# Optimization experiments

Hardware: AMD Instinct MI355X
Metric: run time of the kernel (lower is better)

Reference implementation:

```python
import jax, jax.numpy as jnp
import numpy as np

N_NODES = 50000
N_EDGES = 800000
IN_CH = 128
HIDDEN = 32
HEADS = 4
NEG_SLOPE = 0.2


def segment_softmax(e, seg, num_segments):
    # numerically stable softmax over edges grouped by destination node
    m = jax.ops.segment_max(e, seg, num_segments=num_segments)
    ex = jnp.exp(e - m[seg])
    denom = jax.ops.segment_sum(ex, seg, num_segments=num_segments)
    return ex / denom[seg]


def gat_layer(x, src, dst, W, a_src, a_dst, b, num_nodes, concat):
    H, C = a_src.shape
    h = (x @ W).reshape(num_nodes, H, C)            # (N, H, C)
    alpha_s = jnp.einsum('nhc,hc->nh', h, a_src)    # (N, H)
    alpha_d = jnp.einsum('nhc,hc->nh', h, a_dst)    # (N, H)
    e = jax.nn.leaky_relu(alpha_s[src] + alpha_d[dst], negative_slope=NEG_SLOPE)  # (E, H)
    att = segment_softmax(e, dst, num_nodes)        # (E, H)
    out = jax.ops.segment_sum(h[src] * att[:, :, None], dst, num_segments=num_nodes)  # (N, H, C)
    if concat:
        out = out.reshape(num_nodes, H * C)
    else:
        out = out.mean(axis=1)
    return out + b


def setup_inputs() -> dict:
    key = jax.random.key(0)
    ks = jax.random.split(key, 12)
    s = 0.1
    return {
        'x': jax.random.normal(ks[0], (N_NODES, IN_CH), dtype=jnp.float32),
        'edge_index': jax.random.randint(ks[1], (2, N_EDGES), 0, N_NODES, dtype=jnp.int64),
        'W1': jax.random.normal(ks[2], (IN_CH, HEADS * HIDDEN), dtype=jnp.float32) * s,
        'a_src1': jax.random.normal(ks[3], (HEADS, HIDDEN), dtype=jnp.float32) * s,
        'a_dst1': jax.random.normal(ks[4], (HEADS, HIDDEN), dtype=jnp.float32) * s,
        'b1': jnp.zeros((HEADS * HIDDEN,), dtype=jnp.float32),
        'W2': jax.random.normal(ks[5], (HEADS * HIDDEN, 1 * HIDDEN), dtype=jnp.float32) * s,
        'a_src2': jax.random.normal(ks[6], (1, HIDDEN), dtype=jnp.float32) * s,
        'a_dst2': jax.random.normal(ks[7], (1, HIDDEN), dtype=jnp.float32) * s,
        'b2': jnp.zeros((HIDDEN,), dtype=jnp.float32),
    }


def reference(x, edge_index, W1, a_src1, a_dst1, b1, W2, a_src2, a_dst2, b2):
    n = x.shape[0]
    loops = jnp.arange(n, dtype=edge_index.dtype)
    src = jnp.concatenate([edge_index[0], loops])  # PyG GATConv add_self_loops=True
    dst = jnp.concatenate([edge_index[1], loops])
    h = gat_layer(x, src, dst, W1, a_src1, a_dst1, b1, n, concat=True)
    h = jax.nn.elu(h)  # ELU between layers (dropout=0.0)
    out = gat_layer(h, src, dst, W2, a_src2, a_dst2, b2, n, concat=False)
    return out
```

## Files before the change

### kernel.cpp

```cpp
#include <hip/hip_runtime.h>
#include <cstdint>

#define NEG_SLOPE 0.2f
#define LDA 136
#define PB  256
#define CAP 5120
#define SMEM_BYTES (64 * LDA * 2)

__device__ __forceinline__ float leaky(float v) { return v > 0.f ? v : NEG_SLOPE * v; }
__device__ __forceinline__ float elu(float v) { return v > 0.f ? v : __expf(v) - 1.f; }

typedef _Float16 half2v __attribute__((ext_vector_type(2)));
typedef _Float16 f16x8 __attribute__((ext_vector_type(8)));
typedef float f32x4 __attribute__((ext_vector_type(4)));
union H8 { float4 f4; half2v h[4]; f16x8 v8; };
union H4 { float2 f2; half2v h[2]; };
union HF2 { float2 f2; _Float16 h[4]; };
union HH { f16x8 v; half2v h[4]; };


__device__ __forceinline__ void prep_body(int bid, int G, int tid,
        const float* __restrict__ W1, const float* __restrict__ W2,
        _Float16* __restrict__ W1t, _Float16* __restrict__ W2t) {
    for (int i = bid * 256 + tid; i < 128 * 128; i += G * 256) {
        int c = i >> 7, k = i & 127;
        W1t[i] = (_Float16)W1[k * 128 + c];
    }
    for (int i = bid * 256 + tid; i < 32 * 128; i += G * 256) {
        int c = i >> 7, k = i & 127;
        W2t[i] = (_Float16)W2[k * 32 + c];
    }
}

__device__ __forceinline__ void gemm1_tile(int b, int tid, _Float16* Ah,
        const float* __restrict__ x, const _Float16* __restrict__ W1t,
        const float* __restrict__ a_src, const float* __restrict__ a_dst,
        _Float16* __restrict__ h1h, float* __restrict__ as1, float* __restrict__ ad1,
        int n) {
    int row0 = b * 64;
    const float4* x4 = (const float4*)x;
#pragma unroll
    for (int i = 0; i < 8; ++i) {
        int idx = tid + i * 256;
        int row = idx >> 5, c4 = idx & 31;
        float4 v = make_float4(0.f, 0.f, 0.f, 0.f);
        if (row0 + row < n) v = x4[(size_t)(row0 + row) * 32 + c4];
        HF2 u;
        u.h[0] = (_Float16)v.x; u.h[1] = (_Float16)v.y;
        u.h[2] = (_Float16)v.z; u.h[3] = (_Float16)v.w;
        *(float2*)&Ah[row * LDA + c4 * 4] = u.f2;
    }
    __syncthreads();

    int l = tid & 63, w = tid >> 6;
    int lr = l & 15, lg = l >> 4;
    f16x8 af[4];
#pragma unroll
    for (int kk = 0; kk < 4; ++kk)
        af[kk] = *(const f16x8*)&Ah[(w * 16 + lr) * LDA + kk * 32 + lg * 8];
    f32x4 acc[8];
#pragma unroll
    for (int t = 0; t < 8; ++t) acc[t] = (f32x4)0.f;
#pragma unroll
    for (int t = 0; t < 8; ++t) {
#pragma unroll
        for (int kk = 0; kk < 4; ++kk) {
            f16x8 bf = *(const f16x8*)&W1t[(size_t)(t * 16 + lr) * 128 + kk * 32 + lg * 8];
            acc[t] = __builtin_amdgcn_mfma_f32_16x16x32_f16(af[kk], bf, acc[t], 0, 0, 0);
        }
    }
    __syncthreads();
#pragma unroll
    for (int t = 0; t < 8; ++t)
#pragma unroll
        for (int r = 0; r < 4; ++r)
            Ah[(w * 16 + lg * 4 + r) * LDA + t * 16 + lr] = (_Float16)acc[t][r];
    __syncthreads();
    int row = tid >> 2, q = tid & 3;
    if (row0 + row < n) {
        const float* asv = a_src + q * 32;
        const float* adv = a_dst + q * 32;
        float ps = 0.f, pd = 0.f;
#pragma unroll
        for (int j = 0; j < 4; ++j) {
            f16x8 v = *(const f16x8*)&Ah[row * LDA + q * 32 + j * 8];
            *(f16x8*)&h1h[(size_t)(row0 + row) * 128 + q * 32 + j * 8] = v;
#pragma unroll
            for (int e = 0; e < 8; ++e) {
                float f = (float)v[e];
                ps += f * asv[j * 8 + e];
                pd += f * adv[j * 8 + e];
            }
        }
        as1[(row0 + row) * 4 + q] = ps;
        ad1[(row0 + row) * 4 + q] = pd;
    }
}


__global__ __launch_bounds__(256) void pairprep_kernel(
        const int* __restrict__ src, const int* __restrict__ dstp,
        int* __restrict__ bcur, int2* __restrict__ pairs,
        int E, int NB, int CH,
        const float* __restrict__ W1, const float* __restrict__ W2,
        _Float16* __restrict__ W1t, _Float16* __restrict__ W2t) {
    int bid = (int)blockIdx.x, tid = threadIdx.x;
    if (bid >= PB) {
        prep_body(bid - PB, (int)gridDim.x - PB, tid, W1, W2, W1t, W2t);
        return;
    }
    __shared__ int lh[256];
    for (int t = tid; t < NB; t += 256) lh[t] = 0;
    __syncthreads();
    int e0 = bid * CH, e1 = min(e0 + CH, E);
    int nv = (e1 - e0) & ~3;
    for (int i = e0 + tid * 4; i < e0 + nv; i += 1024) {
        int4 d = *(const int4*)(dstp + i);
        atomicAdd(&lh[d.x >> 8], 1);
        atomicAdd(&lh[d.y >> 8], 1);
        atomicAdd(&lh[d.z >> 8], 1);
        atomicAdd(&lh[d.w >> 8], 1);
    }
    for (int i = e0 + nv + tid; i < e1; i += 256)
        atomicAdd(&lh[dstp[i] >> 8], 1);
    __syncthreads();
    for (int t = tid; t < NB; t += 256) {
        int c = lh[t];
        lh[t] = (c > 0) ? atomicAdd(&bcur[t], c) : 0;
    }
    __syncthreads();
    for (int i = e0 + tid * 4; i < e0 + nv; i += 1024) {
        int4 d = *(const int4*)(dstp + i);
        int4 s = *(const int4*)(src + i);
        int b0 = d.x >> 8, b1 = d.y >> 8, b2 = d.z >> 8, b3 = d.w >> 8;
        int r0 = atomicAdd(&lh[b0], 1);
        int r1 = atomicAdd(&lh[b1], 1);
        int r2 = atomicAdd(&lh[b2], 1);
        int r3 = atomicAdd(&lh[b3], 1);
        if (r0 < CAP) pairs[(size_t)b0 * CAP + r0] = make_int2(s.x, d.x & 255);
        if (r1 < CAP) pairs[(size_t)b1 * CAP + r1] = make_int2(s.y, d.y & 255);
        if (r2 < CAP) pairs[(size_t)b2 * CAP + r2] = make_int2(s.z, d.z & 255);
        if (r3 < CAP) pairs[(size_t)b3 * CAP + r3] = make_int2(s.w, d.w & 255);
    }
    for (int i = e0 + nv + tid; i < e1; i += 256) {
        int d = dstp[i];
        int b = d >> 8;
        int r = atomicAdd(&lh[b], 1);
        if (r < CAP) pairs[(size_t)b * CAP + r] = make_int2(src[i], d & 255);
    }
}

__device__ __forceinline__ void csr_bucket(int b, int tid, unsigned char* smem,
        const int2* __restrict__ pairs, const int* __restrict__ bcur,
        int* __restrict__ rp, int* __restrict__ col, int E, int N, int NB) {
    int* lsz    = (int*)smem;
    int* lstart = lsz + 256;
    int* lnh    = lstart + 256;
    int* lnex   = lnh + 256;
    int* lncur  = lnex + 256;
    int* wsum   = lncur + 256;
    int* woff   = wsum + 4;
    int lane = tid & 63, wv = tid >> 6;

    lsz[tid] = (tid < NB) ? bcur[tid] : 0;
    __syncthreads();
    int v = lsz[tid];
    int x = v;
#pragma unroll
    for (int o = 1; o < 64; o <<= 1) { int u = __shfl_up(x, o); if (lane >= o) x += u; }
    if (lane == 63) wsum[wv] = x;
    __syncthreads();
    if (tid == 0) { int a = 0; for (int i = 0; i < 4; ++i) { woff[i] = a; a += wsum[i]; } }
    __syncthreads();
    lstart[tid] = x - v + woff[wv];
    __syncthreads();

    if (b >= NB) { if (tid == 0) rp[N] = E; return; }
    int myStart = lstart[b];
    int S = lsz[b]; if (S > CAP) S = CAP;
    const int2* pb = pairs + (size_t)b * CAP;

    lnh[tid] = 0;
    __syncthreads();
    for (int i = tid; i < S; i += 256) atomicAdd(&lnh[pb[i].y], 1);
    __syncthreads();
    int v2 = lnh[tid];
    int x2 = v2;
#pragma unroll
    for (int o = 1; o < 64; o <<= 1) { int u = __shfl_up(x2, o); if (lane >= o) x2 += u; }
    if (lane == 63) wsum[wv] = x2;
    __syncthreads();
    if (tid == 0) { int a = 0; for (int i = 0; i < 4; ++i) { woff[i] = a; a += wsum[i]; } }
    __syncthreads();
    int ex2 = x2 - v2 + woff[wv];
    lnex[tid] = ex2;
    lncur[tid] = 0;
    int node = (b << 8) + tid;
    if (node <= N) rp[node] = myStart + ex2;
    __syncthreads();
    for (int i = tid; i < S; i += 256) {
        int2 p = pb[i];
        int r = atomicAdd(&lncur[p.y], 1);
        col[myStart + lnex[p.y] + r] = p.x;
    }
}

__global__ __launch_bounds__(256) void csr_gemm_kernel(
        const int2* __restrict__ pairs, const int* __restrict__ bcur,
        int* __restrict__ rp, int* __restrict__ col, int E, int N, int NB, int KB,
        const float* __restrict__ x, const _Float16* __restrict__ W1t,
        const float* __restrict__ a_src, const float* __restrict__ a_dst,
        _Float16* __restrict__ h1h, float* __restrict__ as1, float* __restrict__ ad1) {
    __shared__ __align__(16) unsigned char smem[SMEM_BYTES];
    int bid = (int)blockIdx.x;
    if (bid < KB) {
        csr_bucket(bid, threadIdx.x, smem, pairs, bcur, rp, col, E, N, NB);
        return;
    }
    gemm1_tile(bid - KB, threadIdx.x, (_Float16*)smem, x, W1t, a_src, a_dst,
               h1h, as1, ad1, N);
}

#define W2S 136

__global__ __launch_bounds__(256) void agg1_kernel(const _Float16* __restrict__ h1h,
                                                   const float4* __restrict__ as1,
                                                   const float4* __restrict__ ad1,
                                                   const int* __restrict__ rp,
                                                   const int* __restrict__ col,
                                                   const float* __restrict__ b1,
                                                   const _Float16* __restrict__ W2t,
                                                   const float* __restrict__ a_src2,
                                                   const float* __restrict__ a_dst2,
                                                   _Float16* __restrict__ h2h,
                                                   float* __restrict__ as2,
                                                   float* __restrict__ ad2, int n) {
    __shared__ float4 s_p[4][64];
    __shared__ _Float16 s_row[4][4][128];
    __shared__ _Float16 sW2[32 * W2S];
    int tid = threadIdx.x;
    for (int e = tid; e < 32 * 16; e += 256) {
        int c = e >> 4, k8 = e & 15;
        *(f16x8*)&sW2[c * W2S + k8 * 8] = *(const f16x8*)&W2t[c * 128 + k8 * 8];
    }
    __syncthreads();

    int wave = tid >> 6, lane = tid & 63;
    int q4 = lane >> 4, l4 = lane & 15;
    int g = l4;
    int head = g >> 2;
    int nid = blockIdx.x * 16 + wave * 4 + q4;
    bool vn = nid < n;
    int nc = vn ? nid : 0;
    float4* sp = s_p[wave];
    int start = rp[nc];
    int end = vn ? rp[nc + 1] : start;
    float4 adn = ad1[nc], asn = as1[nc];
    float sv = (head == 0) ? asn.x + adn.x : (head == 1) ? asn.y + adn.y
             : (head == 2) ? asn.z + adn.z : asn.w + adn.w;
    float psf_h = vn ? __expf(leaky(sv)) : 0.f;
    float dnum = 0.f;
    float4 a0 = make_float4(0.f, 0.f, 0.f, 0.f);
    float4 a1 = a0;
    int lb = lane & 48;

    for (int base = start; base < end; base += 16) {
        int i = base + l4;
        int sidx = 0;
        float4 p = make_float4(0.f, 0.f, 0.f, 0.f);
        if (i < end) {
            sidx = col[i];
            float4 a = as1[sidx];
            p.x = __expf(leaky(a.x + adn.x));
            p.y = __expf(leaky(a.y + adn.y));
            p.z = __expf(leaky(a.z + adn.z));
            p.w = __expf(leaky(a.w + adn.w));
        }
        sp[lane] = p;
        int len = min(16, end - base);
        for (int s = 0; s < len; s += 4) {
            int rem = len - s;
            int sl0 = lb + s;
            int rj0 = __shfl(sidx, sl0);
            float pj0 = ((const float*)&sp[sl0])[head];
            H8 u0 = ((const H8*)(h1h + (size_t)rj0 * 128))[g];

            int sl1 = lb + ((1 < rem) ? s + 1 : s);
            int rj1 = __shfl(sidx, sl1);
            float pj1 = (1 < rem) ? ((const float*)&sp[sl1])[head] : 0.f;
            H8 u1 = ((const H8*)(h1h + (size_t)rj1 * 128))[g];

            int sl2 = lb + ((2 < rem) ? s + 2 : s);
            int rj2 = __shfl(sidx, sl2);
            float pj2 = (2 < rem) ? ((const float*)&sp[sl2])[head] : 0.f;
            H8 u2 = ((const H8*)(h1h + (size_t)rj2 * 128))[g];

            int sl3 = lb + ((3 < rem) ? s + 3 : s);
            int rj3 = __shfl(sidx, sl3);
            float pj3 = (3 < rem) ? ((const float*)&sp[sl3])[head] : 0.f;
            H8 u3 = ((const H8*)(h1h + (size_t)rj3 * 128))[g];

            dnum += pj0; dnum += pj1; dnum += pj2; dnum += pj3;
            a0.x += (float)u0.h[0].x * pj0; a0.y += (float)u0.h[0].y * pj0;
            a0.z += (float)u0.h[1].x * pj0; a0.w += (float)u0.h[1].y * pj0;
            a1.x += (float)u0.h[2].x * pj0; a1.y += (float)u0.h[2].y * pj0;
            a1.z += (float)u0.h[3].x * pj0; a1.w += (float)u0.h[3].y * pj0;

            a0.x += (float)u1.h[0].x * pj1; a0.y += (float)u1.h[0].y * pj1;
            a0.z += (float)u1.h[1].x * pj1; a0.w += (float)u1.h[1].y * pj1;
            a1.x += (float)u1.h[2].x * pj1; a1.y += (float)u1.h[2].y * pj1;
            a1.z += (float)u1.h[3].x * pj1; a1.w += (float)u1.h[3].y * pj1;

            a0.x += (float)u2.h[0].x * pj2; a0.y += (float)u2.h[0].y * pj2;
            a0.z += (float)u2.h[1].x * pj2; a0.w += (float)u2.h[1].y * pj2;
            a1.x += (float)u2.h[2].x * pj2; a1.y += (float)u2.h[2].y * pj2;
            a1.z += (float)u2.h[3].x * pj2; a1.w += (float)u2.h[3].y * pj2;

            a0.x += (float)u3.h[0].x * pj3; a0.y += (float)u3.h[0].y * pj3;
            a0.z += (float)u3.h[1].x * pj3; a0.w += (float)u3.h[1].y * pj3;
            a1.x += (float)u3.h[2].x * pj3; a1.y += (float)u3.h[2].y * pj3;
            a1.z += (float)u3.h[3].x * pj3; a1.w += (float)u3.h[3].y * pj3;
        }
    }
    {
        H8 u = ((const H8*)(h1h + (size_t)nc * 128))[g];
        dnum += psf_h;
        a0.x += (float)u.h[0].x * psf_h; a0.y += (float)u.h[0].y * psf_h;
        a0.z += (float)u.h[1].x * psf_h; a0.w += (float)u.h[1].y * psf_h;
        a1.x += (float)u.h[2].x * psf_h; a1.y += (float)u.h[2].y * psf_h;
        a1.z += (float)u.h[3].x * psf_h; a1.w += (float)u.h[3].y * psf_h;
    }
    if (vn) {
        float inv = __builtin_amdgcn_rcpf(dnum);
        const float4* b4 = (const float4*)b1;
        float4 bb0 = b4[g * 2], bb1 = b4[g * 2 + 1];
        float4 r0 = make_float4(elu(a0.x * inv + bb0.x), elu(a0.y * inv + bb0.y),
                                elu(a0.z * inv + bb0.z), elu(a0.w * inv + bb0.w));
        float4 r1 = make_float4(elu(a1.x * inv + bb1.x), elu(a1.y * inv + bb1.y),
                                elu(a1.z * inv + bb1.z), elu(a1.w * inv + bb1.w));
        H8 o8;
        o8.h[0] = half2v{(_Float16)r0.x, (_Float16)r0.y};
        o8.h[1] = half2v{(_Float16)r0.z, (_Float16)r0.w};
        o8.h[2] = half2v{(_Float16)r1.x, (_Float16)r1.y};
        o8.h[3] = half2v{(_Float16)r1.z, (_Float16)r1.w};
        *(float4*)&s_row[wave][q4][g * 8] = o8.f4;
    }
    int c0 = l4, c1 = l4 + 16;
    float acc2a = 0.f, acc2b = 0.f;
#pragma unroll
    for (int k8 = 0; k8 < 16; ++k8) {
        HH rv, w0, w1;
        rv.v = *(const f16x8*)&s_row[wave][q4][k8 * 8];
        w0.v = *(const f16x8*)&sW2[c0 * W2S + k8 * 8];
        w1.v = *(const f16x8*)&sW2[c1 * W2S + k8 * 8];
#if __has_builtin(__builtin_amdgcn_fdot2)
        acc2a = __builtin_amdgcn_fdot2(rv.h[0], w0.h[0], acc2a, false);
        acc2a = __builtin_amdgcn_fdot2(rv.h[1], w0.h[1], acc2a, false);
        acc2a = __builtin_amdgcn_fdot2(rv.h[2], w0.h[2], acc2a, false);
        acc2a = __builtin_amdgcn_fdot2(rv.h[3], w0.h[3], acc2a, false);
        acc2b = __builtin_amdgcn_fdot2(rv.h[0], w1.h[0], acc2b, false);
        acc2b = __builtin_amdgcn_fdot2(rv.h[1], w1.h[1], acc2b, false);
        acc2b = __builtin_amdgcn_fdot2(rv.h[2], w1.h[2], acc2b, false);
        acc2b = __builtin_amdgcn_fdot2(rv.h[3], w1.h[3], acc2b, false);
#else
#pragma unroll
        for (int e = 0; e < 8; ++e) {
            acc2a += (float)rv.v[e] * (float)w0.v[e];
            acc2b += (float)rv.v[e] * (float)w1.v[e];
        }
#endif
    }
    float ps = acc2a * a_src2[c0] + acc2b * a_src2[c1];
    float pd = acc2a * a_dst2[c0] + acc2b * a_dst2[c1];
#pragma unroll
    for (int o = 1; o < 16; o <<= 1) { ps += __shfl_xor(ps, o); pd += __shfl_xor(pd, o); }
    if (vn) {
        h2h[(size_t)nid * 32 + c0] = (_Float16)acc2a;
        h2h[(size_t)nid * 32 + c1] = (_Float16)acc2b;
        if (l4 == 0) { as2[nid] = ps; ad2[nid] = pd; }
    }
}

__global__ __launch_bounds__(256) void agg2_kernel(const _Float16* __restrict__ h2h,
                                                   const float* __restrict__ as2,
                                                   const float* __restrict__ ad2,
                                                   const int* __restrict__ rp,
                                                   const int* __restrict__ col,
                                                   const float* __restrict__ b2,
                                                   float* __restrict__ out, int n) {
    int wave = threadIdx.x >> 6, lane = threadIdx.x & 63;
    int q8 = lane >> 3, l3 = lane & 7;
    int g = l3;
    int nid = blockIdx.x * 32 + wave * 8 + q8;
    bool vn = nid < n;
    int nc = vn ? nid : 0;
    int start = rp[nc];
    int end = vn ? rp[nc + 1] : start;
    float adn = ad2[nc];
    float psf = vn ? __expf(leaky(as2[nc] + adn)) : 0.f;
    float dnum = 0.f;
    float4 acc = make_float4(0.f, 0.f, 0.f, 0.f);
    int lb = lane & 56;
    for (int base = start; base < end; base += 8) {
        int i = base + l3;
        int sidx = 0;
        float p = 0.f;
        if (i < end) {
            sidx = col[i];
            p = __expf(leaky(as2[sidx] + adn));
        }
        int len = min(8, end - base);
        for (int s = 0; s < len; s += 4) {
            int rem = len - s;
            int sl0 = lb + s;
            int rj0 = __shfl(sidx, sl0);
            float pj0 = __shfl(p, sl0);
            H4 u0 = ((const H4*)(h2h + (size_t)rj0 * 32))[g];

            int sl1 = lb + ((1 < rem) ? s + 1 : s);
            int rj1 = __shfl(sidx, sl1);
            float pj1 = (1 < rem) ? __shfl(p, sl1) : 0.f;
            H4 u1 = ((const H4*)(h2h + (size_t)rj1 * 32))[g];

            int sl2 = lb + ((2 < rem) ? s + 2 : s);
            int rj2 = __shfl(sidx, sl2);
            float pj2 = (2 < rem) ? __shfl(p, sl2) : 0.f;
            H4 u2 = ((const H4*)(h2h + (size_t)rj2 * 32))[g];

            int sl3 = lb + ((3 < rem) ? s + 3 : s);
            int rj3 = __shfl(sidx, sl3);
            float pj3 = (3 < rem) ? __shfl(p, sl3) : 0.f;
            H4 u3 = ((const H4*)(h2h + (size_t)rj3 * 32))[g];

            dnum += pj0; dnum += pj1; dnum += pj2; dnum += pj3;
            acc.x += (float)u0.h[0].x * pj0; acc.y += (float)u0.h[0].y * pj0;
            acc.z += (float)u0.h[1].x * pj0; acc.w += (float)u0.h[1].y * pj0;
            acc.x += (float)u1.h[0].x * pj1; acc.y += (float)u1.h[0].y * pj1;
            acc.z += (float)u1.h[1].x * pj1; acc.w += (float)u1.h[1].y * pj1;
            acc.x += (float)u2.h[0].x * pj2; acc.y += (float)u2.h[0].y * pj2;
            acc.z += (float)u2.h[1].x * pj2; acc.w += (float)u2.h[1].y * pj2;
            acc.x += (float)u3.h[0].x * pj3; acc.y += (float)u3.h[0].y * pj3;
            acc.z += (float)u3.h[1].x * pj3; acc.w += (float)u3.h[1].y * pj3;
        }
    }
    {
        H4 u = ((const H4*)(h2h + (size_t)nc * 32))[g];
        dnum += psf;
        acc.x += (float)u.h[0].x * psf; acc.y += (float)u.h[0].y * psf;
        acc.z += (float)u.h[1].x * psf; acc.w += (float)u.h[1].y * psf;
    }
    if (vn) {
        float inv = __builtin_amdgcn_rcpf(dnum);
        float4 bb = ((const float4*)b2)[g];
        ((float4*)(out + (size_t)nid * 32))[g] =
            make_float4(acc.x * inv + bb.x, acc.y * inv + bb.y,
                        acc.z * inv + bb.z, acc.w * inv + bb.w);
    }
}


extern "C" void kernel_launch(void* const* d_in, const int* in_sizes, int n_in,
                              void* d_out, int out_size, void* d_ws, size_t ws_size,
                              hipStream_t stream) {
    const float* x      = (const float*)d_in[0];
    const int*   ei     = (const int*)d_in[1];
    const float* W1     = (const float*)d_in[2];
    const float* a_src1 = (const float*)d_in[3];
    const float* a_dst1 = (const float*)d_in[4];
    const float* b1     = (const float*)d_in[5];
    const float* W2     = (const float*)d_in[6];
    const float* a_src2 = (const float*)d_in[7];
    const float* a_dst2 = (const float*)d_in[8];
    const float* b2     = (const float*)d_in[9];
    float* out = (float*)d_out;

    const int N = in_sizes[0] / 128;
    const int E = in_sizes[1] / 2;
    const int* src = ei;
    const int* dstp = ei + E;

    uint8_t* w = (uint8_t*)d_ws;
    auto carve = [&](size_t bytes) {
        uint8_t* p = w;
        w += (bytes + 255) & ~(size_t)255;
        return p;
    };
    _Float16* h1h = (_Float16*)carve((size_t)N * 128 * 2);
    _Float16* h2h = (_Float16*)carve((size_t)N * 32 * 2);
    _Float16* W1t = (_Float16*)carve((size_t)128 * 128 * 2);
    _Float16* W2t = (_Float16*)carve((size_t)32 * 128 * 2);
    float* as1 = (float*)carve((size_t)N * 4 * 4);
    float* ad1 = (float*)carve((size_t)N * 4 * 4);
    float* as2 = (float*)carve((size_t)N * 4);
    float* ad2 = (float*)carve((size_t)N * 4);
    int* rp    = (int*)carve((size_t)(N + 1) * 4);
    int* col   = (int*)carve((size_t)E * 4);
    int* bcur  = (int*)carve(256 * 4);

    const int NB = ((N - 1) >> 8) + 1;
    const int KB = (N >> 8) + 1;
    int CH = (E + PB - 1) / PB;
    CH = (CH + 3) & ~3;
    const int gemmBlocks = (N + 63) / 64;
    const int agg1Groups = (N + 15) / 16;
    const int agg2Groups = (N + 31) / 32;

    int2* pairs = (int2*)carve((size_t)NB * CAP * 8);

    hipMemsetAsync(bcur, 0, 256 * 4, stream);
    pairprep_kernel<<<PB + 80, 256, 0, stream>>>(src, dstp, bcur, pairs,
                                                 E, NB, CH, W1, W2, W1t, W2t);
    csr_gemm_kernel<<<KB + gemmBlocks, 256, 0, stream>>>(
        pairs, bcur, rp, col, E, N, NB, KB,
        x, W1t, a_src1, a_dst1, h1h, as1, ad1);
    agg1_kernel<<<agg1Groups, 256, 0, stream>>>(h1h, (const float4*)as1,
                                                (const float4*)ad1, rp, col, b1,
                                                W2t, a_src2, a_dst2, h2h, as2, ad2, N);
    agg2_kernel<<<agg2Groups, 256, 0, stream>>>(h2h, as2, ad2, rp, col, b2, out, N);
}
```

Before: 180.0 us.

## Replace global atomic bucket offsets with per-block fixed-size slots in edge binning

Each pairprep block now writes its edges into a private fixed-capacity slot per destination bucket, and records per-(bucket, block) counts. This removes the separate counting pass, the global atomicAdd on bucket cursors, and the memset launch. The CSR builder sums each bucket's per-block counts to get bucket sizes, and each thread walks one block's slot serially. In exchange, the pairs buffer is larger and the reads in csr_bucket are strided and uncoalesced. Edges beyond 44 per block per bucket would be dropped, though that is unlikely at this degree distribution.

```diff
diff --git a/kernel.cpp b/kernel.cpp
--- a/kernel.cpp
+++ b/kernel.cpp
@@ -3,8 +3,8 @@
 
 #define NEG_SLOPE 0.2f
 #define LDA 136
-#define PB  256
-#define CAP 5120
+#define PB   256
+#define SLOT 44
 #define SMEM_BYTES (64 * LDA * 2)
 
 __device__ __forceinline__ float leaky(float v) { return v > 0.f ? v : NEG_SLOPE * v; }
@@ -100,7 +100,7 @@
 
 __global__ __launch_bounds__(256) void pairprep_kernel(
         const int* __restrict__ src, const int* __restrict__ dstp,
-        int* __restrict__ bcur, int2* __restrict__ pairs,
+        int* __restrict__ cnt, int2* __restrict__ pairs,
         int E, int NB, int CH,
         const float* __restrict__ W1, const float* __restrict__ W2,
         _Float16* __restrict__ W1t, _Float16* __restrict__ W2t) {
@@ -114,21 +114,6 @@
     __syncthreads();
     int e0 = bid * CH, e1 = min(e0 + CH, E);
     int nv = (e1 - e0) & ~3;
-    for (int i = e0 + tid * 4; i < e0 + nv; i += 1024) {
-        int4 d = *(const int4*)(dstp + i);
-        atomicAdd(&lh[d.x >> 8], 1);
-        atomicAdd(&lh[d.y >> 8], 1);
-        atomicAdd(&lh[d.z >> 8], 1);
-        atomicAdd(&lh[d.w >> 8], 1);
-    }
-    for (int i = e0 + nv + tid; i < e1; i += 256)
-        atomicAdd(&lh[dstp[i] >> 8], 1);
-    __syncthreads();
-    for (int t = tid; t < NB; t += 256) {
-        int c = lh[t];
-        lh[t] = (c > 0) ? atomicAdd(&bcur[t], c) : 0;
-    }
-    __syncthreads();
     for (int i = e0 + tid * 4; i < e0 + nv; i += 1024) {
         int4 d = *(const int4*)(dstp + i);
         int4 s = *(const int4*)(src + i);
@@ -137,21 +122,23 @@
         int r1 = atomicAdd(&lh[b1], 1);
         int r2 = atomicAdd(&lh[b2], 1);
         int r3 = atomicAdd(&lh[b3], 1);
-        if (r0 < CAP) pairs[(size_t)b0 * CAP + r0] = make_int2(s.x, d.x & 255);
-        if (r1 < CAP) pairs[(size_t)b1 * CAP + r1] = make_int2(s.y, d.y & 255);
-        if (r2 < CAP) pairs[(size_t)b2 * CAP + r2] = make_int2(s.z, d.z & 255);
-        if (r3 < CAP) pairs[(size_t)b3 * CAP + r3] = make_int2(s.w, d.w & 255);
+        if (r0 < SLOT) pairs[((size_t)b0 * PB + bid) * SLOT + r0] = make_int2(s.x, d.x & 255);
+        if (r1 < SLOT) pairs[((size_t)b1 * PB + bid) * SLOT + r1] = make_int2(s.y, d.y & 255);
+        if (r2 < SLOT) pairs[((size_t)b2 * PB + bid) * SLOT + r2] = make_int2(s.z, d.z & 255);
+        if (r3 < SLOT) pairs[((size_t)b3 * PB + bid) * SLOT + r3] = make_int2(s.w, d.w & 255);
     }
     for (int i = e0 + nv + tid; i < e1; i += 256) {
         int d = dstp[i];
         int b = d >> 8;
         int r = atomicAdd(&lh[b], 1);
-        if (r < CAP) pairs[(size_t)b * CAP + r] = make_int2(src[i], d & 255);
-    }
+        if (r < SLOT) pairs[((size_t)b * PB + bid) * SLOT + r] = make_int2(src[i], d & 255);
+    }
+    __syncthreads();
+    for (int t = tid; t < NB; t += 256) cnt[t * PB + bid] = min(lh[t], SLOT);
 }
 
 __device__ __forceinline__ void csr_bucket(int b, int tid, unsigned char* smem,
-        const int2* __restrict__ pairs, const int* __restrict__ bcur,
+        const int2* __restrict__ pairs, const int* __restrict__ cnt,
         int* __restrict__ rp, int* __restrict__ col, int E, int N, int NB) {
     int* lsz    = (int*)smem;
     int* lstart = lsz + 256;
@@ -162,7 +149,15 @@
     int* woff   = wsum + 4;
     int lane = tid & 63, wv = tid >> 6;
 
-    lsz[tid] = (tid < NB) ? bcur[tid] : 0;
+    {
+        int s = 0;
+        if (tid < NB) {
+            const int4* row = (const int4*)(cnt + tid * PB);
+#pragma unroll 8
+            for (int i = 0; i < PB / 4; ++i) { int4 v = row[i]; s += v.x + v.y + v.z + v.w; }
+        }
+        lsz[tid] = s;
+    }
     __syncthreads();
     int v = lsz[tid];
     int x = v;
@@ -175,14 +170,17 @@
     lstart[tid] = x - v + woff[wv];
     __syncthreads();
 
-    if (b >= NB) { if (tid == 0) rp[N] = E; return; }
+    if (b >= NB) {
+        if (tid == 0) rp[N] = lstart[NB - 1] + lsz[NB - 1];
+        return;
+    }
     int myStart = lstart[b];
-    int S = lsz[b]; if (S > CAP) S = CAP;
-    const int2* pb = pairs + (size_t)b * CAP;
+    int k = cnt[b * PB + tid];
+    const int2* pc = pairs + ((size_t)b * PB + tid) * SLOT;
 
     lnh[tid] = 0;
     __syncthreads();
-    for (int i = tid; i < S; i += 256) atomicAdd(&lnh[pb[i].y], 1);
+    for (int i = 0; i < k; ++i) atomicAdd(&lnh[pc[i].y], 1);
     __syncthreads();
     int v2 = lnh[tid];
     int x2 = v2;
@@ -198,15 +196,15 @@
     int node = (b << 8) + tid;
     if (node <= N) rp[node] = myStart + ex2;
     __syncthreads();
-    for (int i = tid; i < S; i += 256) {
-        int2 p = pb[i];
+    for (int i = 0; i < k; ++i) {
+        int2 p = pc[i];
         int r = atomicAdd(&lncur[p.y], 1);
         col[myStart + lnex[p.y] + r] = p.x;
     }
 }
 
 __global__ __launch_bounds__(256) void csr_gemm_kernel(
-        const int2* __restrict__ pairs, const int* __restrict__ bcur,
+        const int2* __restrict__ pairs, const int* __restrict__ cnt,
         int* __restrict__ rp, int* __restrict__ col, int E, int N, int NB, int KB,
         const float* __restrict__ x, const _Float16* __restrict__ W1t,
         const float* __restrict__ a_src, const float* __restrict__ a_dst,
@@ -214,7 +212,7 @@
     __shared__ __align__(16) unsigned char smem[SMEM_BYTES];
     int bid = (int)blockIdx.x;
     if (bid < KB) {
-        csr_bucket(bid, threadIdx.x, smem, pairs, bcur, rp, col, E, N, NB);
+        csr_bucket(bid, threadIdx.x, smem, pairs, cnt, rp, col, E, N, NB);
         return;
     }
     gemm1_tile(bid - KB, threadIdx.x, (_Float16*)smem, x, W1t, a_src, a_dst,
@@ -495,7 +493,7 @@
     float* ad2 = (float*)carve((size_t)N * 4);
     int* rp    = (int*)carve((size_t)(N + 1) * 4);
     int* col   = (int*)carve((size_t)E * 4);
-    int* bcur  = (int*)carve(256 * 4);
+    int* cnt   = (int*)carve((size_t)256 * PB * 4);
 
     const int NB = ((N - 1) >> 8) + 1;
     const int KB = (N >> 8) + 1;
@@ -505,13 +503,12 @@
     const int agg1Groups = (N + 15) / 16;
     const int agg2Groups = (N + 31) / 32;
 
-    int2* pairs = (int2*)carve((size_t)NB * CAP * 8);
-
-    hipMemsetAsync(bcur, 0, 256 * 4, stream);
-    pairprep_kernel<<<PB + 80, 256, 0, stream>>>(src, dstp, bcur, pairs,
+    int2* pairs = (int2*)carve((size_t)NB * PB * SLOT * 8);
+
+    pairprep_kernel<<<PB + 80, 256, 0, stream>>>(src, dstp, cnt, pairs,
                                                  E, NB, CH, W1, W2, W1t, W2t);
     csr_gemm_kernel<<<KB + gemmBlocks, 256, 0, stream>>>(
-        pairs, bcur, rp, col, E, N, NB, KB,
+        pairs, cnt, rp, col, E, N, NB, KB,
         x, W1t, a_src1, a_dst1, h1h, as1, ad1);
     agg1_kernel<<<agg1Groups, 256, 0, stream>>>(h1h, (const float4*)as1,
                                                 (const float4*)ad1, rp, col, b1,
```

New measurement: 182.5 us. No clear change (+1.4%).
